# Kernel tuning notes

Hardware: AMD Instinct MI355X
Metric: run time of the kernel (lower is better)

Reference implementation:

```python
import jax, jax.numpy as jnp
import numpy as np

N_POWER_ITER = 5


def _spectral_normalize(w, n_iter=N_POWER_ITER):
    # w: [out, in] 1x1-conv weight; divide by top singular value (power iteration,
    # deterministic init), mirroring torch.nn.utils.spectral_norm's reparameterization.
    u = jnp.full((w.shape[0],), 1.0 / np.sqrt(w.shape[0]), dtype=w.dtype)
    for _ in range(n_iter):
        v = w.T @ u
        v = v / (jnp.linalg.norm(v) + 1e-12)
        u = w @ v
        u = u / (jnp.linalg.norm(u) + 1e-12)
    sigma = u @ (w @ v)
    return w / sigma


def _maxpool2x2(x):
    # x: [B, C, H, W] -> [B, C, H//2, W//2]
    B, C, H, W = x.shape
    return x.reshape(B, C, H // 2, 2, W // 2, 2).max(axis=(3, 5))


def _conv1x1(w, x):
    # 1x1 conv == channel-mixing einsum. w: [out, in], x: [B, in, H, W]
    return jnp.einsum('oc,bchw->bohw', w, x)


def setup_inputs() -> dict:
    key = jax.random.key(0)
    kx, kq, kk, kv, ko = jax.random.split(key, 5)
    C = 512
    B, H, W = 16, 64, 64
    scale = 0.05
    return {
        'x': jax.random.normal(kx, (B, C, H, W), dtype=jnp.float32),
        'Wq': jax.random.normal(kq, (C // 8, C), dtype=jnp.float32) * scale,
        'Wk': jax.random.normal(kk, (C // 8, C), dtype=jnp.float32) * scale,
        'Wv': jax.random.normal(kv, (C // 2, C), dtype=jnp.float32) * scale,
        'Wo': jax.random.normal(ko, (C, C // 2), dtype=jnp.float32) * scale,
        'gamma': jnp.array([0.5], dtype=jnp.float32),
    }


def reference(x, Wq, Wk, Wv, Wo, gamma):
    B, C, H, W = x.shape
    n_ftrs = H * W
    wq = _spectral_normalize(Wq)
    wk = _spectral_normalize(Wk)
    wv = _spectral_normalize(Wv)
    wo = _spectral_normalize(Wo)
    f = _conv1x1(wq, x).reshape(B, C // 8, n_ftrs)                      # [B, C/8, HW]
    g = _maxpool2x2(_conv1x1(wk, x)).reshape(B, C // 8, n_ftrs // 4)    # [B, C/8, HW/4]
    h = _maxpool2x2(_conv1x1(wv, x)).reshape(B, C // 2, n_ftrs // 4)    # [B, C/2, HW/4]
    # scores: [B, HW, HW/4]; softmax over kv positions
    beta = jax.nn.softmax(jnp.einsum('bcn,bcm->bnm', f, g), axis=-1)
    # attention output: [B, C/2, HW]
    o = jnp.einsum('bcm,bnm->bcn', h, beta).reshape(B, C // 2, H, W)
    o = _conv1x1(wo, o)                                                 # [B, C, H, W]
    return gamma.reshape(()) * o + x
```

## Files before the change

### kernel.cpp

```cpp
#include <hip/hip_runtime.h>
#include <cstdint>

typedef __attribute__((ext_vector_type(8))) short bf16x8;
typedef __attribute__((ext_vector_type(4))) float f32x4;
typedef __attribute__((ext_vector_type(2))) unsigned int u32x2;

#define B_   16
#define C_   512
#define HW_  4096
#define M3_  384
#define HWP_ 1024
#define CV_  256

__device__ __forceinline__ unsigned short f2b(float f) {
  union { float f; unsigned u; } v; v.f = f;
  unsigned r = v.u + 0x7fffu + ((v.u >> 16) & 1u);
  return (unsigned short)(r >> 16);
}
__device__ __forceinline__ float b2f(unsigned short b) {
  union { unsigned u; float f; } v; v.u = ((unsigned)b) << 16;
  return v.f;
}
__device__ __forceinline__ f32x4 mfma16(bf16x8 a, bf16x8 b, f32x4 c) {
  return __builtin_amdgcn_mfma_f32_16x16x32_bf16(a, b, c, 0, 0, 0);
}

__global__ __launch_bounds__(256) void k_transpose(const float* __restrict__ x,
                                                   unsigned short* __restrict__ xb) {
  __shared__ unsigned short t[64][66];
  const int b = blockIdx.z, k0 = blockIdx.y * 64, n0 = blockIdx.x * 64;
  const float* xp = x + (size_t)b * C_ * HW_;
  const int ln = threadIdx.x & 63, g = threadIdx.x >> 6;
  for (int kk = g; kk < 64; kk += 4)
    t[kk][ln] = f2b(xp[(size_t)(k0 + kk) * HW_ + n0 + ln]);
  __syncthreads();
  unsigned short* xo = xb + (size_t)b * HW_ * C_;
  for (int nn = g; nn < 64; nn += 4)
    xo[(size_t)(n0 + nn) * C_ + k0 + ln] = t[ln][nn];
}

__global__ __launch_bounds__(256) void k_wtrans(
    const float* __restrict__ Wq, const float* __restrict__ Wk,
    const float* __restrict__ Wv, const float* __restrict__ Wo,
    float* __restrict__ wt) {
  const float* w; int out, in; float* dst;
  switch (blockIdx.z) {
    case 0: w = Wq; out = 64;  in = 512; dst = wt;          break;
    case 1: w = Wk; out = 64;  in = 512; dst = wt + 32768;  break;
    case 2: w = Wv; out = 256; in = 512; dst = wt + 65536;  break;
    default: w = Wo; out = 512; in = 256; dst = wt + 196608; break;
  }
  const int o0 = blockIdx.y * 64, i0 = blockIdx.x * 64;
  if (o0 >= out || i0 >= in) return;
  __shared__ float t[64][65];
  const int ln = threadIdx.x & 63, g = threadIdx.x >> 6;
  for (int oo = g; oo < 64; oo += 4)
    t[oo][ln] = w[(size_t)(o0 + oo) * in + i0 + ln];
  __syncthreads();
  for (int ii = g; ii < 64; ii += 4)
    dst[(size_t)(i0 + ii) * out + o0 + ln] = t[ln][ii];
}

__device__ __forceinline__ float breduce1024(float val, float* red) {
  __syncthreads();
#pragma unroll
  for (int off = 32; off > 0; off >>= 1) val += __shfl_down(val, off);
  if ((threadIdx.x & 63) == 0) red[threadIdx.x >> 6] = val;
  __syncthreads();
  float s = 0.f;
#pragma unroll
  for (int i = 0; i < 16; ++i) s += red[i];
  return s;
}

__global__ __launch_bounds__(1024) void k_specnorm(
    const float* __restrict__ Wq, const float* __restrict__ Wk,
    const float* __restrict__ Wv, const float* __restrict__ Wo,
    const float* __restrict__ wt,
    unsigned short* __restrict__ wqkv, unsigned short* __restrict__ wob) {
  __shared__ float u[512], v[512];
  __shared__ float part[4096];
  __shared__ float red[16];
  const float* w; const float* wT; int out, in; unsigned short* dst;
  switch (blockIdx.x) {
    case 0: w = Wq; wT = wt;          out = 64;  in = 512; dst = wqkv;             break;
    case 1: w = Wk; wT = wt + 32768;  out = 64;  in = 512; dst = wqkv + 64 * 512;  break;
    case 2: w = Wv; wT = wt + 65536;  out = 256; in = 512; dst = wqkv + 128 * 512; break;
    default: w = Wo; wT = wt + 196608; out = 512; in = 256; dst = wob;             break;
  }
  const int tid = threadIdx.x;
  const float rs = rsqrtf((float)out);
  if (tid < out) u[tid] = rs;
  __syncthreads();
  for (int it = 0; it < 5; ++it) {
    {
      const int G = in >> 2, nch = 1024 / G;
      const int ch = tid / G, grp = tid - ch * G;
      const int rpc = out / nch, obase = ch * rpc;
      f32x4 acc = {0.f, 0.f, 0.f, 0.f};
#pragma unroll 8
      for (int r = 0; r < rpc; ++r) {
        const int o = obase + r;
        const f32x4 wv = *reinterpret_cast<const f32x4*>(&w[(size_t)o * in + grp * 4]);
        const float uo = u[o];
        acc[0] += wv[0] * uo; acc[1] += wv[1] * uo;
        acc[2] += wv[2] * uo; acc[3] += wv[3] * uo;
      }
      *reinterpret_cast<f32x4*>(&part[ch * in + grp * 4]) = acc;
      __syncthreads();
      if (tid < in) {
        float s = 0.f;
        for (int c2 = 0; c2 < nch; ++c2) s += part[c2 * in + tid];
        v[tid] = s;
      }
    }
    {
      float ss = (tid < in) ? 0.f : 0.f;
      if (tid < in) { __syncthreads(); ss = v[tid] * v[tid]; } else { __syncthreads(); }
      ss = breduce1024(ss, red);
      const float sv = 1.f / (sqrtf(ss) + 1e-12f);
      if (tid < in) v[tid] *= sv;
      __syncthreads();
    }
    {
      const int G = out >> 2, nch = 1024 / G;
      const int ch = tid / G, grp = tid - ch * G;
      const int cpc = in / nch, cbase = ch * cpc;
      f32x4 acc = {0.f, 0.f, 0.f, 0.f};
#pragma unroll 8
      for (int r = 0; r < cpc; ++r) {
        const int c = cbase + r;
        const f32x4 wv = *reinterpret_cast<const f32x4*>(&wT[(size_t)c * out + grp * 4]);
        const float vc = v[c];
        acc[0] += wv[0] * vc; acc[1] += wv[1] * vc;
        acc[2] += wv[2] * vc; acc[3] += wv[3] * vc;
      }
      *reinterpret_cast<f32x4*>(&part[ch * out + grp * 4]) = acc;
      __syncthreads();
      if (tid < out) {
        float s = 0.f;
        for (int c2 = 0; c2 < nch; ++c2) s += part[c2 * out + tid];
        u[tid] = s;
      }
    }
    {
      float su = 0.f;
      __syncthreads();
      if (tid < out) su = u[tid] * u[tid];
      su = breduce1024(su, red);
      const float sv2 = 1.f / (sqrtf(su) + 1e-12f);
      if (tid < out) u[tid] *= sv2;
      __syncthreads();
    }
  }
  float sp = 0.f;
  {
    const int G = out >> 2, nch = 1024 / G;
    const int ch = tid / G, grp = tid - ch * G;
    const int cpc = in / nch, cbase = ch * cpc;
    f32x4 acc = {0.f, 0.f, 0.f, 0.f};
#pragma unroll 8
    for (int r = 0; r < cpc; ++r) {
      const int c = cbase + r;
      const f32x4 wv = *reinterpret_cast<const f32x4*>(&wT[(size_t)c * out + grp * 4]);
      const float vc = v[c];
      acc[0] += wv[0] * vc; acc[1] += wv[1] * vc;
      acc[2] += wv[2] * vc; acc[3] += wv[3] * vc;
    }
    *reinterpret_cast<f32x4*>(&part[ch * out + grp * 4]) = acc;
    __syncthreads();
    if (tid < out) {
      float s = 0.f;
      for (int c2 = 0; c2 < nch; ++c2) s += part[c2 * out + tid];
      sp = s * u[tid];
    }
  }
  sp = breduce1024(sp, red);
  const float oscale = (blockIdx.x == 0) ? 1.44269504f : 1.0f;
  const float inv_sigma = (1.f / sp) * oscale;
  const int total = out * in;
  for (int i = tid * 4; i < total; i += 4096) {
    const f32x4 wv = *reinterpret_cast<const f32x4*>(&w[i]);
    u32x2 pw;
    pw[0] = ((unsigned)f2b(wv[1] * inv_sigma) << 16) | f2b(wv[0] * inv_sigma);
    pw[1] = ((unsigned)f2b(wv[3] * inv_sigma) << 16) | f2b(wv[2] * inv_sigma);
    *reinterpret_cast<u32x2*>(&dst[i]) = pw;
  }
}

__global__ __launch_bounds__(256) void k_gemm_qkv(
    const unsigned short* __restrict__ xb, const unsigned short* __restrict__ wqkv,
    unsigned short* __restrict__ yt) {
  __shared__ alignas(16) char smem[32768];
  unsigned short* As = (unsigned short*)smem;
  unsigned short* Bs = (unsigned short*)(smem + 16384);
  const int lid = blockIdx.x;
  const int swz = (lid & 7) * 192 + (lid >> 3);
  const int mt = swz % 3, rest = swz / 3;
  const int nt = rest & 31, b = rest >> 5;
  const int n0 = nt * 128, m0 = mt * 128;
  const unsigned short* Ap = xb + (size_t)b * HW_ * C_ + (size_t)n0 * C_;
  const unsigned short* Bp = wqkv + (size_t)m0 * C_;
  const int tid = threadIdx.x, lane = tid & 63, wid = tid >> 6;
  const int wn = (wid >> 1) * 64, wm = (wid & 1) * 64;
  f32x4 acc[4][4] = {};
  for (int k0 = 0; k0 < C_; k0 += 64) {
    __syncthreads();
#pragma unroll
    for (int i = 0; i < 4; ++i) {
      const int r = i * 32 + (tid >> 3);
      const int s = tid & 7, ss = s ^ (r & 7);
      *reinterpret_cast<f32x4*>(&As[r * 64 + ss * 8]) =
          *reinterpret_cast<const f32x4*>(&Ap[(size_t)r * C_ + k0 + s * 8]);
      *reinterpret_cast<f32x4*>(&Bs[r * 64 + ss * 8]) =
          *reinterpret_cast<const f32x4*>(&Bp[(size_t)r * C_ + k0 + s * 8]);
    }
    __syncthreads();
#pragma unroll
    for (int kk = 0; kk < 2; ++kk) {
      bf16x8 af[4], bfr[4];
#pragma unroll
      for (int i = 0; i < 4; ++i) {
        const int r = wn + i * 16 + (lane & 15);
        const int slot = (kk * 4 + (lane >> 4)) ^ (r & 7);
        af[i] = *reinterpret_cast<const bf16x8*>(&As[r * 64 + slot * 8]);
      }
#pragma unroll
      for (int j = 0; j < 4; ++j) {
        const int r = wm + j * 16 + (lane & 15);
        const int slot = (kk * 4 + (lane >> 4)) ^ (r & 7);
        bfr[j] = *reinterpret_cast<const bf16x8*>(&Bs[r * 64 + slot * 8]);
      }
#pragma unroll
      for (int i = 0; i < 4; ++i)
#pragma unroll
        for (int j = 0; j < 4; ++j) acc[i][j] = mfma16(af[i], bfr[j], acc[i][j]);
    }
  }
  unsigned short* eps = (unsigned short*)smem;
  unsigned short* Y = yt + (size_t)b * HW_ * M3_;
#pragma unroll
  for (int h = 0; h < 2; ++h) {
    __syncthreads();
    if ((wid >> 1) == h) {
#pragma unroll
      for (int i = 0; i < 4; ++i)
#pragma unroll
        for (int j = 0; j < 4; ++j)
#pragma unroll
          for (int r = 0; r < 4; ++r) {
            const int nl = i * 16 + (lane >> 4) * 4 + r;
            const int ml = wm + j * 16 + (lane & 15);
            eps[nl * 136 + ml] = f2b(acc[i][j][r]);
          }
    }
    __syncthreads();
#pragma unroll
    for (int t = 0; t < 4; ++t) {
      const int row = t * 16 + (tid >> 4);
      const int m8 = (tid & 15) * 8;
      *reinterpret_cast<f32x4*>(&Y[(size_t)(n0 + h * 64 + row) * M3_ + m0 + m8]) =
          *reinterpret_cast<const f32x4*>(&eps[row * 136 + m8]);
    }
  }
}

__global__ __launch_bounds__(256) void k_pool_g(const unsigned short* __restrict__ yt,
                                                unsigned short* __restrict__ gt) {
  const int b = blockIdx.y, mp0 = blockIdx.x * 64;
  const int c = threadIdx.x & 63, dm = threadIdx.x >> 6;
  const unsigned short* Y = yt + (size_t)b * HW_ * M3_;
  unsigned short* G = gt + (size_t)b * HWP_ * 64;
  for (int mm = dm; mm < 64; mm += 4) {
    const int mp = mp0 + mm;
    const int n00 = (mp >> 5) * 128 + (mp & 31) * 2;
    const float a0 = b2f(Y[(size_t)n00 * M3_ + 64 + c]);
    const float a1 = b2f(Y[(size_t)(n00 + 1) * M3_ + 64 + c]);
    const float a2 = b2f(Y[(size_t)(n00 + 64) * M3_ + 64 + c]);
    const float a3 = b2f(Y[(size_t)(n00 + 65) * M3_ + 64 + c]);
    G[(size_t)mp * 64 + c] = f2b(fmaxf(fmaxf(a0, a1), fmaxf(a2, a3)));
  }
}

__global__ __launch_bounds__(256) void k_pool_vt(const unsigned short* __restrict__ yt,
                                                 unsigned short* __restrict__ vt) {
  __shared__ unsigned short t[64][66];
  const int b = blockIdx.z, mp0 = blockIdx.x * 64, cv0 = blockIdx.y * 64;
  const unsigned short* Y = yt + (size_t)b * HW_ * M3_;
  const int c = threadIdx.x & 63, dm = threadIdx.x >> 6;
  for (int mm = dm; mm < 64; mm += 4) {
    const int mp = mp0 + mm;
    const int n00 = (mp >> 5) * 128 + (mp & 31) * 2;
    const float a0 = b2f(Y[(size_t)n00 * M3_ + 128 + cv0 + c]);
    const float a1 = b2f(Y[(size_t)(n00 + 1) * M3_ + 128 + cv0 + c]);
    const float a2 = b2f(Y[(size_t)(n00 + 64) * M3_ + 128 + cv0 + c]);
    const float a3 = b2f(Y[(size_t)(n00 + 65) * M3_ + 128 + cv0 + c]);
    t[mm][c] = f2b(fmaxf(fmaxf(a0, a1), fmaxf(a2, a3)));
  }
  __syncthreads();
  unsigned short* V = vt + (size_t)b * CV_ * HWP_;
  for (int cc = dm; cc < 64; cc += 4)
    V[(size_t)(cv0 + cc) * HWP_ + mp0 + c] = t[c][cc];
}

__global__ __launch_bounds__(512, 4) void k_attn(
    const unsigned short* __restrict__ yt, const unsigned short* __restrict__ gt,
    const unsigned short* __restrict__ vt, unsigned short* __restrict__ oat) {
  __shared__ alignas(16) char smem[57344];
  unsigned short* Ks = (unsigned short*)smem;
  unsigned short* Vs = (unsigned short*)(smem + 8192);
  unsigned short* Ps = (unsigned short*)(smem + 40960);
  const int lid = blockIdx.x;
  const int swz = (lid & 7) * 64 + (lid >> 3);
  const int q0 = (swz & 31) * 128, b = swz >> 5;
  const int tid = threadIdx.x, lane = tid & 63, wid = tid >> 6;
  const int q = lane & 15, g = lane >> 4;
  const unsigned short* Qg = yt + (size_t)b * HW_ * M3_ + (size_t)q0 * M3_;
  const unsigned short* Gg = gt + (size_t)b * HWP_ * 64;
  const unsigned short* Vg = vt + (size_t)b * CV_ * HWP_;
  unsigned short* P = Ps + wid * 1024;
  bf16x8 qf[2];
#pragma unroll
  for (int kk = 0; kk < 2; ++kk)
    qf[kk] = *reinterpret_cast<const bf16x8*>(&Qg[(size_t)(wid * 16 + q) * M3_ + kk * 32 + g * 8]);
  f32x4 kreg, vreg[4];
  {
    const int r = tid >> 3, s = tid & 7;
    kreg = *reinterpret_cast<const f32x4*>(&Gg[(size_t)r * 64 + s * 8]);
  }
#pragma unroll
  for (int t = 0; t < 4; ++t) {
    const int ch = tid + t * 512, r = ch >> 3, s = ch & 7;
    vreg[t] = *reinterpret_cast<const f32x4*>(&Vg[(size_t)r * HWP_ + s * 8]);
  }
  f32x4 oacc[16] = {};
  float m_run = -1e30f, l_run = 0.f;
  for (int it = 0; it < 16; ++it) {
    __syncthreads();
    {
      const int r = tid >> 3, s = tid & 7, ss = s ^ (r & 7);
      *reinterpret_cast<f32x4*>(&Ks[r * 64 + ss * 8]) = kreg;
    }
#pragma unroll
    for (int t = 0; t < 4; ++t) {
      const int ch = tid + t * 512, r = ch >> 3, s = ch & 7, ss = s ^ (r & 7);
      *reinterpret_cast<f32x4*>(&Vs[r * 64 + ss * 8]) = vreg[t];
    }
    __syncthreads();
    if (it < 15) {
      const int kvn = (it + 1) * 64;
      {
        const int r = tid >> 3, s = tid & 7;
        kreg = *reinterpret_cast<const f32x4*>(&Gg[(size_t)(kvn + r) * 64 + s * 8]);
      }
#pragma unroll
      for (int t = 0; t < 4; ++t) {
        const int ch = tid + t * 512, r = ch >> 3, s = ch & 7;
        vreg[t] = *reinterpret_cast<const f32x4*>(&Vg[(size_t)r * HWP_ + kvn + s * 8]);
      }
    }
    f32x4 sacc[4] = {};
#pragma unroll
    for (int kk = 0; kk < 2; ++kk) {
      bf16x8 kf[4];
#pragma unroll
      for (int i = 0; i < 4; ++i) {
        const int row = i * 16 + q;
        const int sl = (kk * 4 + g) ^ (row & 7);
        kf[i] = *reinterpret_cast<const bf16x8*>(&Ks[row * 64 + sl * 8]);
      }
#pragma unroll
      for (int i = 0; i < 4; ++i) sacc[i] = mfma16(kf[i], qf[kk], sacc[i]);
    }
    float tmax = -1e30f;
#pragma unroll
    for (int i = 0; i < 4; ++i)
#pragma unroll
      for (int r = 0; r < 4; ++r) tmax = fmaxf(tmax, sacc[i][r]);
    tmax = fmaxf(tmax, __shfl_xor(tmax, 16));
    tmax = fmaxf(tmax, __shfl_xor(tmax, 32));
    if (__any(tmax > m_run + 11.0f)) {
      const float mnew = fmaxf(m_run, tmax);
      const float alpha = exp2f(m_run - mnew);
      m_run = mnew;
      l_run *= alpha;
      float al[4];
#pragma unroll
      for (int r = 0; r < 4; ++r) al[r] = __shfl(alpha, g * 4 + r);
#pragma unroll
      for (int j = 0; j < 16; ++j) {
        oacc[j][0] *= al[0]; oacc[j][1] *= al[1];
        oacc[j][2] *= al[2]; oacc[j][3] *= al[3];
      }
    }
    float lsum = 0.f;
#pragma unroll
    for (int i = 0; i < 4; ++i) {
      const float p0 = exp2f(sacc[i][0] - m_run);
      const float p1 = exp2f(sacc[i][1] - m_run);
      const float p2 = exp2f(sacc[i][2] - m_run);
      const float p3 = exp2f(sacc[i][3] - m_run);
      lsum += (p0 + p1) + (p2 + p3);
      u32x2 pw;
      pw[0] = ((unsigned)f2b(p1) << 16) | f2b(p0);
      pw[1] = ((unsigned)f2b(p3) << 16) | f2b(p2);
      const int sl = (2 * i + (g >> 1)) ^ (q & 7);
      *reinterpret_cast<u32x2*>(&P[q * 64 + sl * 8 + (g & 1) * 4]) = pw;
    }
    lsum += __shfl_xor(lsum, 16);
    lsum += __shfl_xor(lsum, 32);
    l_run += lsum;
    __builtin_amdgcn_s_setprio(1);
#pragma unroll
    for (int kk = 0; kk < 2; ++kk) {
      const bf16x8 pa = *reinterpret_cast<const bf16x8*>(&P[q * 64 + ((kk * 4 + g) ^ (q & 7)) * 8]);
#pragma unroll
      for (int j = 0; j < 16; ++j) {
        const int row = j * 16 + q;
        const int sl = (kk * 4 + g) ^ (row & 7);
        const bf16x8 vf = *reinterpret_cast<const bf16x8*>(&Vs[row * 64 + sl * 8]);
        oacc[j] = mfma16(pa, vf, oacc[j]);
      }
    }
    __builtin_amdgcn_s_setprio(0);
  }
  float linv[4];
  {
    const float myinv = 1.f / l_run;
#pragma unroll
    for (int r = 0; r < 4; ++r) linv[r] = __shfl(myinv, g * 4 + r);
  }
  unsigned short* eps = (unsigned short*)smem;
  unsigned short* O = oat + (size_t)b * HW_ * CV_ + (size_t)q0 * CV_;
#pragma unroll
  for (int h = 0; h < 2; ++h) {
    __syncthreads();
    if ((wid >> 2) == h) {
#pragma unroll
      for (int j = 0; j < 16; ++j)
#pragma unroll
        for (int r = 0; r < 4; ++r) {
          const int row = (wid & 3) * 16 + g * 4 + r;
          const int cv = j * 16 + q;
          eps[row * 264 + cv] = f2b(oacc[j][r] * linv[r]);
        }
    }
    __syncthreads();
#pragma unroll
    for (int t = 0; t < 4; ++t) {
      const int row = t * 16 + (tid >> 5);
      const int cv8 = (tid & 31) * 8;
      *reinterpret_cast<f32x4*>(&O[(size_t)(h * 64 + row) * CV_ + cv8]) =
          *reinterpret_cast<const f32x4*>(&eps[row * 264 + cv8]);
    }
  }
}

__global__ __launch_bounds__(256) void k_gemm_out(
    const unsigned short* __restrict__ oat, const unsigned short* __restrict__ wob,
    const float* __restrict__ x, const float* __restrict__ gamma,
    float* __restrict__ out) {
  __shared__ alignas(16) char smem[32768];
  unsigned short* As = (unsigned short*)smem;
  unsigned short* Bs = (unsigned short*)(smem + 16384);
  const int lid = blockIdx.x;
  const int swz = (lid & 7) * 256 + (lid >> 3);
  const int ct = swz & 3, nt = (swz >> 2) & 31, b = swz >> 7;
  const int n0 = nt * 128, co0 = ct * 128;
  const unsigned short* Ap = wob + (size_t)co0 * CV_;
  const unsigned short* Bp = oat + (size_t)b * HW_ * CV_ + (size_t)n0 * CV_;
  const int tid = threadIdx.x, lane = tid & 63, wid = tid >> 6;
  const int wc = (wid >> 1) * 64, wn = (wid & 1) * 64;
  f32x4 acc[4][4] = {};
  for (int k0 = 0; k0 < CV_; k0 += 64) {
    __syncthreads();
#pragma unroll
    for (int i = 0; i < 4; ++i) {
      const int r = i * 32 + (tid >> 3);
      const int s = tid & 7, ss = s ^ (r & 7);
      *reinterpret_cast<f32x4*>(&As[r * 64 + ss * 8]) =
          *reinterpret_cast<const f32x4*>(&Ap[(size_t)r * CV_ + k0 + s * 8]);
      *reinterpret_cast<f32x4*>(&Bs[r * 64 + ss * 8]) =
          *reinterpret_cast<const f32x4*>(&Bp[(size_t)r * CV_ + k0 + s * 8]);
    }
    __syncthreads();
#pragma unroll
    for (int kk = 0; kk < 2; ++kk) {
      bf16x8 af[4], bfr[4];
#pragma unroll
      for (int i = 0; i < 4; ++i) {
        const int r = wc + i * 16 + (lane & 15);
        const int slot = (kk * 4 + (lane >> 4)) ^ (r & 7);
        af[i] = *reinterpret_cast<const bf16x8*>(&As[r * 64 + slot * 8]);
      }
#pragma unroll
      for (int j = 0; j < 4; ++j) {
        const int r = wn + j * 16 + (lane & 15);
        const int slot = (kk * 4 + (lane >> 4)) ^ (r & 7);
        bfr[j] = *reinterpret_cast<const bf16x8*>(&Bs[r * 64 + slot * 8]);
      }
#pragma unroll
      for (int i = 0; i < 4; ++i)
#pragma unroll
        for (int j = 0; j < 4; ++j) acc[i][j] = mfma16(af[i], bfr[j], acc[i][j]);
    }
  }
  float* eps = (float*)smem;
  const float g = gamma[0];
  const size_t base = (size_t)b * C_ * HW_;
#pragma unroll
  for (int h = 0; h < 4; ++h) {
    __syncthreads();
    if ((wid >> 1) == (h >> 1)) {
#pragma unroll
      for (int ii = 0; ii < 2; ++ii) {
        const int i = (h & 1) * 2 + ii;
#pragma unroll
        for (int j = 0; j < 4; ++j)
#pragma unroll
          for (int r = 0; r < 4; ++r) {
            const int col2 = ii * 16 + (lane >> 4) * 4 + r;
            const int nl = wn + j * 16 + (lane & 15);
            eps[col2 * 132 + nl] = acc[i][j][r];
          }
      }
    }
    __syncthreads();
#pragma unroll
    for (int t = 0; t < 4; ++t) {
      const int row = t * 8 + (tid >> 5);
      const int col = (tid & 31) * 4;
      const size_t goff = base + (size_t)(co0 + h * 32 + row) * HW_ + n0 + col;
      const f32x4 xv = *reinterpret_cast<const f32x4*>(&x[goff]);
      const f32x4 av = *reinterpret_cast<const f32x4*>(&eps[row * 132 + col]);
      f32x4 ov;
      ov[0] = g * av[0] + xv[0];
      ov[1] = g * av[1] + xv[1];
      ov[2] = g * av[2] + xv[2];
      ov[3] = g * av[3] + xv[3];
      *reinterpret_cast<f32x4*>(&out[goff]) = ov;
    }
  }
}

extern "C" void kernel_launch(void* const* d_in, const int* in_sizes, int n_in,
                              void* d_out, int out_size, void* d_ws, size_t ws_size,
                              hipStream_t stream) {
  (void)in_sizes; (void)n_in; (void)out_size; (void)ws_size;
  const float* x     = (const float*)d_in[0];
  const float* Wq    = (const float*)d_in[1];
  const float* Wk    = (const float*)d_in[2];
  const float* Wv    = (const float*)d_in[3];
  const float* Wo    = (const float*)d_in[4];
  const float* gamma = (const float*)d_in[5];
  float* out = (float*)d_out;
  char* ws = (char*)d_ws;

  unsigned short* wqkv = (unsigned short*)(ws);
  unsigned short* wob  = (unsigned short*)(ws + 393216);
  unsigned short* xb   = (unsigned short*)(ws + 655360);
  unsigned short* yt   = (unsigned short*)(ws + 67764224);
  unsigned short* gt   = (unsigned short*)(ws + 118095872);
  unsigned short* vt   = (unsigned short*)(ws + 120193024);
  unsigned short* oat  = xb;
  float* wt = (float*)yt;

  k_transpose<<<dim3(64, 8, 16), 256, 0, stream>>>(x, xb);
  k_wtrans<<<dim3(8, 8, 4), 256, 0, stream>>>(Wq, Wk, Wv, Wo, wt);
  k_specnorm<<<4, 1024, 0, stream>>>(Wq, Wk, Wv, Wo, wt, wqkv, wob);
  k_gemm_qkv<<<1536, 256, 0, stream>>>(xb, wqkv, yt);
  k_pool_g<<<dim3(16, 16), 256, 0, stream>>>(yt, gt);
  k_pool_vt<<<dim3(16, 4, 16), 256, 0, stream>>>(yt, vt);
  k_attn<<<512, 512, 0, stream>>>(yt, gt, vt, oat);
  k_gemm_out<<<2048, 256, 0, stream>>>(oat, wob, x, gamma, out);
}
```

Before: 349.1 us.

## Restructure attention kernel to split value channels across waves with register-resident K/V

The attention kernel now uses 256-thread blocks, each handling 64 queries. Each wave owns 64 value channels for all 64 queries rather than 16 queries across all 256 channels. K and V fragments load straight from global memory into registers, with prefetch of the next tile, so the LDS staging of K/V and two barriers per iteration are gone. P tiles and per-row rescale factors are shared through double-buffered LDS with one barrier per iteration. In exchange every block reloads K redundantly, the grid doubles, and occupancy shifts (launch bounds 256,3). A small specnorm barrier cleanup is also included.

```diff
diff --git a/kernel.cpp b/kernel.cpp
--- a/kernel.cpp
+++ b/kernel.cpp
@@ -115,8 +115,9 @@
       }
     }
     {
-      float ss = (tid < in) ? 0.f : 0.f;
-      if (tid < in) { __syncthreads(); ss = v[tid] * v[tid]; } else { __syncthreads(); }
+      float ss = 0.f;
+      __syncthreads();
+      if (tid < in) ss = v[tid] * v[tid];
       ss = breduce1024(ss, red);
       const float sv = 1.f / (sqrtf(ss) + 1e-12f);
       if (tid < in) v[tid] *= sv;
@@ -303,74 +304,53 @@
     V[(size_t)(cv0 + cc) * HWP_ + mp0 + c] = t[c][cc];
 }
 
-__global__ __launch_bounds__(512, 4) void k_attn(
+__global__ __launch_bounds__(256, 3) void k_attn(
     const unsigned short* __restrict__ yt, const unsigned short* __restrict__ gt,
     const unsigned short* __restrict__ vt, unsigned short* __restrict__ oat) {
-  __shared__ alignas(16) char smem[57344];
-  unsigned short* Ks = (unsigned short*)smem;
-  unsigned short* Vs = (unsigned short*)(smem + 8192);
-  unsigned short* Ps = (unsigned short*)(smem + 40960);
+  __shared__ alignas(16) char smem[34048];
+  float* aLds = (float*)(smem + 16384);
+  int* fLds = (int*)(smem + 16896);
   const int lid = blockIdx.x;
-  const int swz = (lid & 7) * 64 + (lid >> 3);
-  const int q0 = (swz & 31) * 128, b = swz >> 5;
+  const int swz = (lid & 7) * 128 + (lid >> 3);
+  const int q0 = (swz & 63) * 64, b = swz >> 6;
   const int tid = threadIdx.x, lane = tid & 63, wid = tid >> 6;
   const int q = lane & 15, g = lane >> 4;
+  const int cvb = wid * 64;
   const unsigned short* Qg = yt + (size_t)b * HW_ * M3_ + (size_t)q0 * M3_;
   const unsigned short* Gg = gt + (size_t)b * HWP_ * 64;
-  const unsigned short* Vg = vt + (size_t)b * CV_ * HWP_;
-  unsigned short* P = Ps + wid * 1024;
+  const unsigned short* Vg = vt + (size_t)b * CV_ * HWP_ + (size_t)cvb * HWP_;
   bf16x8 qf[2];
 #pragma unroll
   for (int kk = 0; kk < 2; ++kk)
     qf[kk] = *reinterpret_cast<const bf16x8*>(&Qg[(size_t)(wid * 16 + q) * M3_ + kk * 32 + g * 8]);
-  f32x4 kreg, vreg[4];
-  {
-    const int r = tid >> 3, s = tid & 7;
-    kreg = *reinterpret_cast<const f32x4*>(&Gg[(size_t)r * 64 + s * 8]);
-  }
-#pragma unroll
-  for (int t = 0; t < 4; ++t) {
-    const int ch = tid + t * 512, r = ch >> 3, s = ch & 7;
-    vreg[t] = *reinterpret_cast<const f32x4*>(&Vg[(size_t)r * HWP_ + s * 8]);
-  }
-  f32x4 oacc[16] = {};
+  bf16x8 kf[2][4], vf[2][4];
+#pragma unroll
+  for (int kk = 0; kk < 2; ++kk)
+#pragma unroll
+    for (int i = 0; i < 4; ++i)
+      kf[kk][i] = *reinterpret_cast<const bf16x8*>(&Gg[(size_t)(i * 16 + q) * 64 + kk * 32 + g * 8]);
+#pragma unroll
+  for (int kk = 0; kk < 2; ++kk)
+#pragma unroll
+    for (int j = 0; j < 4; ++j)
+      vf[kk][j] = *reinterpret_cast<const bf16x8*>(&Vg[(size_t)(j * 16 + q) * HWP_ + kk * 32 + g * 8]);
+  f32x4 oacc[4][4] = {};
   float m_run = -1e30f, l_run = 0.f;
   for (int it = 0; it < 16; ++it) {
-    __syncthreads();
-    {
-      const int r = tid >> 3, s = tid & 7, ss = s ^ (r & 7);
-      *reinterpret_cast<f32x4*>(&Ks[r * 64 + ss * 8]) = kreg;
-    }
-#pragma unroll
-    for (int t = 0; t < 4; ++t) {
-      const int ch = tid + t * 512, r = ch >> 3, s = ch & 7, ss = s ^ (r & 7);
-      *reinterpret_cast<f32x4*>(&Vs[r * 64 + ss * 8]) = vreg[t];
-    }
-    __syncthreads();
+    const int cur = it & 1;
+    unsigned short* P = (unsigned short*)smem + cur * 4096;
+    f32x4 sacc[4] = {};
+#pragma unroll
+    for (int kk = 0; kk < 2; ++kk)
+#pragma unroll
+      for (int i = 0; i < 4; ++i) sacc[i] = mfma16(kf[kk][i], qf[kk], sacc[i]);
     if (it < 15) {
       const int kvn = (it + 1) * 64;
-      {
-        const int r = tid >> 3, s = tid & 7;
-        kreg = *reinterpret_cast<const f32x4*>(&Gg[(size_t)(kvn + r) * 64 + s * 8]);
-      }
-#pragma unroll
-      for (int t = 0; t < 4; ++t) {
-        const int ch = tid + t * 512, r = ch >> 3, s = ch & 7;
-        vreg[t] = *reinterpret_cast<const f32x4*>(&Vg[(size_t)r * HWP_ + kvn + s * 8]);
-      }
-    }
-    f32x4 sacc[4] = {};
-#pragma unroll
-    for (int kk = 0; kk < 2; ++kk) {
-      bf16x8 kf[4];
-#pragma unroll
-      for (int i = 0; i < 4; ++i) {
-        const int row = i * 16 + q;
-        const int sl = (kk * 4 + g) ^ (row & 7);
-        kf[i] = *reinterpret_cast<const bf16x8*>(&Ks[row * 64 + sl * 8]);
-      }
-#pragma unroll
-      for (int i = 0; i < 4; ++i) sacc[i] = mfma16(kf[i], qf[kk], sacc[i]);
+#pragma unroll
+      for (int kk = 0; kk < 2; ++kk)
+#pragma unroll
+        for (int i = 0; i < 4; ++i)
+          kf[kk][i] = *reinterpret_cast<const bf16x8*>(&Gg[(size_t)(kvn + i * 16 + q) * 64 + kk * 32 + g * 8]);
     }
     float tmax = -1e30f;
 #pragma unroll
@@ -379,20 +359,18 @@
       for (int r = 0; r < 4; ++r) tmax = fmaxf(tmax, sacc[i][r]);
     tmax = fmaxf(tmax, __shfl_xor(tmax, 16));
     tmax = fmaxf(tmax, __shfl_xor(tmax, 32));
+    float alpha = 1.f;
+    int resc = 0;
     if (__any(tmax > m_run + 11.0f)) {
       const float mnew = fmaxf(m_run, tmax);
-      const float alpha = exp2f(m_run - mnew);
+      alpha = exp2f(m_run - mnew);
       m_run = mnew;
       l_run *= alpha;
-      float al[4];
-#pragma unroll
-      for (int r = 0; r < 4; ++r) al[r] = __shfl(alpha, g * 4 + r);
-#pragma unroll
-      for (int j = 0; j < 16; ++j) {
-        oacc[j][0] *= al[0]; oacc[j][1] *= al[1];
-        oacc[j][2] *= al[2]; oacc[j][3] *= al[3];
-      }
-    }
+      resc = 1;
+    }
+    if (lane < 16) aLds[cur * 64 + wid * 16 + lane] = alpha;
+    if (lane == 0) fLds[cur * 4 + wid] = resc;
+    const int qg = wid * 16 + q;
     float lsum = 0.f;
 #pragma unroll
     for (int i = 0; i < 4; ++i) {
@@ -405,54 +383,75 @@
       pw[0] = ((unsigned)f2b(p1) << 16) | f2b(p0);
       pw[1] = ((unsigned)f2b(p3) << 16) | f2b(p2);
       const int sl = (2 * i + (g >> 1)) ^ (q & 7);
-      *reinterpret_cast<u32x2*>(&P[q * 64 + sl * 8 + (g & 1) * 4]) = pw;
+      *reinterpret_cast<u32x2*>(&P[qg * 64 + sl * 8 + (g & 1) * 4]) = pw;
     }
     lsum += __shfl_xor(lsum, 16);
     lsum += __shfl_xor(lsum, 32);
     l_run += lsum;
+    __syncthreads();
+    if (fLds[cur * 4 + 0] | fLds[cur * 4 + 1] | fLds[cur * 4 + 2] | fLds[cur * 4 + 3]) {
+#pragma unroll
+      for (int f = 0; f < 4; ++f) {
+        float al[4];
+#pragma unroll
+        for (int r = 0; r < 4; ++r) al[r] = aLds[cur * 64 + f * 16 + g * 4 + r];
+#pragma unroll
+        for (int j = 0; j < 4; ++j) {
+          oacc[f][j][0] *= al[0]; oacc[f][j][1] *= al[1];
+          oacc[f][j][2] *= al[2]; oacc[f][j][3] *= al[3];
+        }
+      }
+    }
     __builtin_amdgcn_s_setprio(1);
 #pragma unroll
     for (int kk = 0; kk < 2; ++kk) {
-      const bf16x8 pa = *reinterpret_cast<const bf16x8*>(&P[q * 64 + ((kk * 4 + g) ^ (q & 7)) * 8]);
-#pragma unroll
-      for (int j = 0; j < 16; ++j) {
-        const int row = j * 16 + q;
-        const int sl = (kk * 4 + g) ^ (row & 7);
-        const bf16x8 vf = *reinterpret_cast<const bf16x8*>(&Vs[row * 64 + sl * 8]);
-        oacc[j] = mfma16(pa, vf, oacc[j]);
+#pragma unroll
+      for (int f = 0; f < 4; ++f) {
+        const int row = f * 16 + q;
+        const bf16x8 pa = *reinterpret_cast<const bf16x8*>(
+            &P[row * 64 + (((kk * 4 + g) ^ (q & 7))) * 8]);
+#pragma unroll
+        for (int j = 0; j < 4; ++j)
+          oacc[f][j] = mfma16(pa, vf[kk][j], oacc[f][j]);
       }
     }
     __builtin_amdgcn_s_setprio(0);
-  }
-  float linv[4];
-  {
-    const float myinv = 1.f / l_run;
-#pragma unroll
-    for (int r = 0; r < 4; ++r) linv[r] = __shfl(myinv, g * 4 + r);
-  }
+    if (it < 15) {
+      const int kvn = (it + 1) * 64;
+#pragma unroll
+      for (int kk = 0; kk < 2; ++kk)
+#pragma unroll
+        for (int j = 0; j < 4; ++j)
+          vf[kk][j] = *reinterpret_cast<const bf16x8*>(&Vg[(size_t)(j * 16 + q) * HWP_ + kvn + kk * 32 + g * 8]);
+    }
+  }
+  float* lLds = (float*)(smem + 33792);
+  if (lane < 16) lLds[wid * 16 + lane] = 1.f / l_run;
+  __syncthreads();
+  float linv[4][4];
+#pragma unroll
+  for (int f = 0; f < 4; ++f)
+#pragma unroll
+    for (int r = 0; r < 4; ++r) linv[f][r] = lLds[f * 16 + g * 4 + r];
   unsigned short* eps = (unsigned short*)smem;
+#pragma unroll
+  for (int f = 0; f < 4; ++f)
+#pragma unroll
+    for (int j = 0; j < 4; ++j)
+#pragma unroll
+      for (int r = 0; r < 4; ++r) {
+        const int row = f * 16 + g * 4 + r;
+        const int cv = cvb + j * 16 + q;
+        eps[row * 264 + cv] = f2b(oacc[f][j][r] * linv[f][r]);
+      }
+  __syncthreads();
   unsigned short* O = oat + (size_t)b * HW_ * CV_ + (size_t)q0 * CV_;
 #pragma unroll
-  for (int h = 0; h < 2; ++h) {
-    __syncthreads();
-    if ((wid >> 2) == h) {
-#pragma unroll
-      for (int j = 0; j < 16; ++j)
-#pragma unroll
-        for (int r = 0; r < 4; ++r) {
-          const int row = (wid & 3) * 16 + g * 4 + r;
-          const int cv = j * 16 + q;
-          eps[row * 264 + cv] = f2b(oacc[j][r] * linv[r]);
-        }
-    }
-    __syncthreads();
-#pragma unroll
-    for (int t = 0; t < 4; ++t) {
-      const int row = t * 16 + (tid >> 5);
-      const int cv8 = (tid & 31) * 8;
-      *reinterpret_cast<f32x4*>(&O[(size_t)(h * 64 + row) * CV_ + cv8]) =
-          *reinterpret_cast<const f32x4*>(&eps[row * 264 + cv8]);
-    }
+  for (int t = 0; t < 8; ++t) {
+    const int row = t * 8 + (tid >> 5);
+    const int cv8 = (tid & 31) * 8;
+    *reinterpret_cast<f32x4*>(&O[(size_t)row * CV_ + cv8]) =
+        *reinterpret_cast<const f32x4*>(&eps[row * 264 + cv8]);
   }
 }
 
@@ -571,6 +570,6 @@
   k_gemm_qkv<<<1536, 256, 0, stream>>>(xb, wqkv, yt);
   k_pool_g<<<dim3(16, 16), 256, 0, stream>>>(yt, gt);
   k_pool_vt<<<dim3(16, 4, 16), 256, 0, stream>>>(yt, vt);
-  k_attn<<<512, 512, 0, stream>>>(yt, gt, vt, oat);
+  k_attn<<<1024, 256, 0, stream>>>(yt, gt, vt, oat);
   k_gemm_out<<<2048, 256, 0, stream>>>(oat, wob, x, gamma, out);
 }
```

Measured after the change: 476.8 us. 1.37x slower.

## Process two query sub-tiles per wave in attention to reuse V fragments

Applied to the files above, without the earlier changes.

The attention kernel now runs 4 waves of 256 threads instead of 8, with each wave handling 32 query rows as two 16-row halves. Each V fragment read from shared memory then feeds two MFMAs, which halves LDS traffic per FLOP and doubles per-thread global staging loads. The cost is about double the accumulator registers (two sets of 16 f32x4 accumulators plus 8 V staging registers), which may lower occupancy or cause spills, and fewer waves per block hide less latency. A redundant conditional __syncthreads in the spectral-norm kernel is also simplified.

```diff
diff --git a/kernel.cpp b/kernel.cpp
--- a/kernel.cpp
+++ b/kernel.cpp
@@ -115,8 +115,9 @@
       }
     }
     {
-      float ss = (tid < in) ? 0.f : 0.f;
-      if (tid < in) { __syncthreads(); ss = v[tid] * v[tid]; } else { __syncthreads(); }
+      float ss = 0.f;
+      __syncthreads();
+      if (tid < in) ss = v[tid] * v[tid];
       ss = breduce1024(ss, red);
       const float sv = 1.f / (sqrtf(ss) + 1e-12f);
       if (tid < in) v[tid] *= sv;
@@ -303,7 +304,7 @@
     V[(size_t)(cv0 + cc) * HWP_ + mp0 + c] = t[c][cc];
 }
 
-__global__ __launch_bounds__(512, 4) void k_attn(
+__global__ __launch_bounds__(256, 2) void k_attn(
     const unsigned short* __restrict__ yt, const unsigned short* __restrict__ gt,
     const unsigned short* __restrict__ vt, unsigned short* __restrict__ oat) {
   __shared__ alignas(16) char smem[57344];
@@ -315,51 +316,56 @@
   const int q0 = (swz & 31) * 128, b = swz >> 5;
   const int tid = threadIdx.x, lane = tid & 63, wid = tid >> 6;
   const int q = lane & 15, g = lane >> 4;
-  const unsigned short* Qg = yt + (size_t)b * HW_ * M3_ + (size_t)q0 * M3_;
+  const unsigned short* Qg = yt + (size_t)b * HW_ * M3_ + (size_t)(q0 + wid * 32) * M3_;
   const unsigned short* Gg = gt + (size_t)b * HWP_ * 64;
   const unsigned short* Vg = vt + (size_t)b * CV_ * HWP_;
-  unsigned short* P = Ps + wid * 1024;
-  bf16x8 qf[2];
-#pragma unroll
-  for (int kk = 0; kk < 2; ++kk)
-    qf[kk] = *reinterpret_cast<const bf16x8*>(&Qg[(size_t)(wid * 16 + q) * M3_ + kk * 32 + g * 8]);
-  f32x4 kreg, vreg[4];
-  {
-    const int r = tid >> 3, s = tid & 7;
-    kreg = *reinterpret_cast<const f32x4*>(&Gg[(size_t)r * 64 + s * 8]);
-  }
-#pragma unroll
-  for (int t = 0; t < 4; ++t) {
-    const int ch = tid + t * 512, r = ch >> 3, s = ch & 7;
+  unsigned short* P = Ps + wid * 2048;
+  bf16x8 qf[2][2];
+#pragma unroll
+  for (int h = 0; h < 2; ++h)
+#pragma unroll
+    for (int kk = 0; kk < 2; ++kk)
+      qf[h][kk] = *reinterpret_cast<const bf16x8*>(&Qg[(size_t)(h * 16 + q) * M3_ + kk * 32 + g * 8]);
+  f32x4 kreg[2], vreg[8];
+#pragma unroll
+  for (int t = 0; t < 2; ++t) {
+    const int i = tid + t * 256, r = i >> 3, s = i & 7;
+    kreg[t] = *reinterpret_cast<const f32x4*>(&Gg[(size_t)r * 64 + s * 8]);
+  }
+#pragma unroll
+  for (int t = 0; t < 8; ++t) {
+    const int i = tid + t * 256, r = i >> 3, s = i & 7;
     vreg[t] = *reinterpret_cast<const f32x4*>(&Vg[(size_t)r * HWP_ + s * 8]);
   }
-  f32x4 oacc[16] = {};
-  float m_run = -1e30f, l_run = 0.f;
+  f32x4 oacc[2][16] = {};
+  float m_run[2] = {-1e30f, -1e30f}, l_run[2] = {0.f, 0.f};
   for (int it = 0; it < 16; ++it) {
     __syncthreads();
-    {
-      const int r = tid >> 3, s = tid & 7, ss = s ^ (r & 7);
-      *reinterpret_cast<f32x4*>(&Ks[r * 64 + ss * 8]) = kreg;
-    }
-#pragma unroll
-    for (int t = 0; t < 4; ++t) {
-      const int ch = tid + t * 512, r = ch >> 3, s = ch & 7, ss = s ^ (r & 7);
+#pragma unroll
+    for (int t = 0; t < 2; ++t) {
+      const int i = tid + t * 256, r = i >> 3, s = i & 7, ss = s ^ (r & 7);
+      *reinterpret_cast<f32x4*>(&Ks[r * 64 + ss * 8]) = kreg[t];
+    }
+#pragma unroll
+    for (int t = 0; t < 8; ++t) {
+      const int i = tid + t * 256, r = i >> 3, s = i & 7, ss = s ^ (r & 7);
       *reinterpret_cast<f32x4*>(&Vs[r * 64 + ss * 8]) = vreg[t];
     }
     __syncthreads();
     if (it < 15) {
       const int kvn = (it + 1) * 64;
-      {
-        const int r = tid >> 3, s = tid & 7;
-        kreg = *reinterpret_cast<const f32x4*>(&Gg[(size_t)(kvn + r) * 64 + s * 8]);
-      }
-#pragma unroll
-      for (int t = 0; t < 4; ++t) {
-        const int ch = tid + t * 512, r = ch >> 3, s = ch & 7;
+#pragma unroll
+      for (int t = 0; t < 2; ++t) {
+        const int i = tid + t * 256, r = i >> 3, s = i & 7;
+        kreg[t] = *reinterpret_cast<const f32x4*>(&Gg[(size_t)(kvn + r) * 64 + s * 8]);
+      }
+#pragma unroll
+      for (int t = 0; t < 8; ++t) {
+        const int i = tid + t * 256, r = i >> 3, s = i & 7;
         vreg[t] = *reinterpret_cast<const f32x4*>(&Vg[(size_t)r * HWP_ + kvn + s * 8]);
       }
     }
-    f32x4 sacc[4] = {};
+    f32x4 sacc[2][4] = {};
 #pragma unroll
     for (int kk = 0; kk < 2; ++kk) {
       bf16x8 kf[4];
@@ -370,87 +376,101 @@
         kf[i] = *reinterpret_cast<const bf16x8*>(&Ks[row * 64 + sl * 8]);
       }
 #pragma unroll
-      for (int i = 0; i < 4; ++i) sacc[i] = mfma16(kf[i], qf[kk], sacc[i]);
-    }
-    float tmax = -1e30f;
-#pragma unroll
-    for (int i = 0; i < 4; ++i)
-#pragma unroll
-      for (int r = 0; r < 4; ++r) tmax = fmaxf(tmax, sacc[i][r]);
-    tmax = fmaxf(tmax, __shfl_xor(tmax, 16));
-    tmax = fmaxf(tmax, __shfl_xor(tmax, 32));
-    if (__any(tmax > m_run + 11.0f)) {
-      const float mnew = fmaxf(m_run, tmax);
-      const float alpha = exp2f(m_run - mnew);
-      m_run = mnew;
-      l_run *= alpha;
-      float al[4];
-#pragma unroll
-      for (int r = 0; r < 4; ++r) al[r] = __shfl(alpha, g * 4 + r);
-#pragma unroll
-      for (int j = 0; j < 16; ++j) {
-        oacc[j][0] *= al[0]; oacc[j][1] *= al[1];
-        oacc[j][2] *= al[2]; oacc[j][3] *= al[3];
-      }
-    }
-    float lsum = 0.f;
-#pragma unroll
-    for (int i = 0; i < 4; ++i) {
-      const float p0 = exp2f(sacc[i][0] - m_run);
-      const float p1 = exp2f(sacc[i][1] - m_run);
-      const float p2 = exp2f(sacc[i][2] - m_run);
-      const float p3 = exp2f(sacc[i][3] - m_run);
-      lsum += (p0 + p1) + (p2 + p3);
-      u32x2 pw;
-      pw[0] = ((unsigned)f2b(p1) << 16) | f2b(p0);
-      pw[1] = ((unsigned)f2b(p3) << 16) | f2b(p2);
-      const int sl = (2 * i + (g >> 1)) ^ (q & 7);
-      *reinterpret_cast<u32x2*>(&P[q * 64 + sl * 8 + (g & 1) * 4]) = pw;
-    }
-    lsum += __shfl_xor(lsum, 16);
-    lsum += __shfl_xor(lsum, 32);
-    l_run += lsum;
+      for (int h = 0; h < 2; ++h)
+#pragma unroll
+        for (int i = 0; i < 4; ++i) sacc[h][i] = mfma16(kf[i], qf[h][kk], sacc[h][i]);
+    }
+#pragma unroll
+    for (int h = 0; h < 2; ++h) {
+      float tmax = -1e30f;
+#pragma unroll
+      for (int i = 0; i < 4; ++i)
+#pragma unroll
+        for (int r = 0; r < 4; ++r) tmax = fmaxf(tmax, sacc[h][i][r]);
+      tmax = fmaxf(tmax, __shfl_xor(tmax, 16));
+      tmax = fmaxf(tmax, __shfl_xor(tmax, 32));
+      if (__any(tmax > m_run[h] + 11.0f)) {
+        const float mnew = fmaxf(m_run[h], tmax);
+        const float alpha = exp2f(m_run[h] - mnew);
+        m_run[h] = mnew;
+        l_run[h] *= alpha;
+        float al[4];
+#pragma unroll
+        for (int r = 0; r < 4; ++r) al[r] = __shfl(alpha, g * 4 + r);
+#pragma unroll
+        for (int j = 0; j < 16; ++j) {
+          oacc[h][j][0] *= al[0]; oacc[h][j][1] *= al[1];
+          oacc[h][j][2] *= al[2]; oacc[h][j][3] *= al[3];
+        }
+      }
+      const int qg = h * 16 + q;
+      float lsum = 0.f;
+#pragma unroll
+      for (int i = 0; i < 4; ++i) {
+        const float p0 = exp2f(sacc[h][i][0] - m_run[h]);
+        const float p1 = exp2f(sacc[h][i][1] - m_run[h]);
+        const float p2 = exp2f(sacc[h][i][2] - m_run[h]);
+        const float p3 = exp2f(sacc[h][i][3] - m_run[h]);
+        lsum += (p0 + p1) + (p2 + p3);
+        u32x2 pw;
+        pw[0] = ((unsigned)f2b(p1) << 16) | f2b(p0);
+        pw[1] = ((unsigned)f2b(p3) << 16) | f2b(p2);
+        const int sl = (2 * i + (g >> 1)) ^ (qg & 7);
+        *reinterpret_cast<u32x2*>(&P[qg * 64 + sl * 8 + (g & 1) * 4]) = pw;
+      }
+      lsum += __shfl_xor(lsum, 16);
+      lsum += __shfl_xor(lsum, 32);
+      l_run[h] += lsum;
+    }
     __builtin_amdgcn_s_setprio(1);
 #pragma unroll
     for (int kk = 0; kk < 2; ++kk) {
-      const bf16x8 pa = *reinterpret_cast<const bf16x8*>(&P[q * 64 + ((kk * 4 + g) ^ (q & 7)) * 8]);
+      bf16x8 pa[2];
+#pragma unroll
+      for (int h = 0; h < 2; ++h)
+        pa[h] = *reinterpret_cast<const bf16x8*>(
+            &P[(h * 16 + q) * 64 + (((kk * 4 + g) ^ (q & 7))) * 8]);
 #pragma unroll
       for (int j = 0; j < 16; ++j) {
         const int row = j * 16 + q;
         const int sl = (kk * 4 + g) ^ (row & 7);
         const bf16x8 vf = *reinterpret_cast<const bf16x8*>(&Vs[row * 64 + sl * 8]);
-        oacc[j] = mfma16(pa, vf, oacc[j]);
+        oacc[0][j] = mfma16(pa[0], vf, oacc[0][j]);
+        oacc[1][j] = mfma16(pa[1], vf, oacc[1][j]);
       }
     }
     __builtin_amdgcn_s_setprio(0);
   }
-  float linv[4];
-  {
-    const float myinv = 1.f / l_run;
-#pragma unroll
-    for (int r = 0; r < 4; ++r) linv[r] = __shfl(myinv, g * 4 + r);
+  float linv[2][4];
+#pragma unroll
+  for (int h = 0; h < 2; ++h) {
+    const float myinv = 1.f / l_run[h];
+#pragma unroll
+    for (int r = 0; r < 4; ++r) linv[h][r] = __shfl(myinv, g * 4 + r);
   }
   unsigned short* eps = (unsigned short*)smem;
   unsigned short* O = oat + (size_t)b * HW_ * CV_ + (size_t)q0 * CV_;
 #pragma unroll
-  for (int h = 0; h < 2; ++h) {
-    __syncthreads();
-    if ((wid >> 2) == h) {
-#pragma unroll
-      for (int j = 0; j < 16; ++j)
-#pragma unroll
-        for (int r = 0; r < 4; ++r) {
-          const int row = (wid & 3) * 16 + g * 4 + r;
-          const int cv = j * 16 + q;
-          eps[row * 264 + cv] = f2b(oacc[j][r] * linv[r]);
-        }
-    }
-    __syncthreads();
-#pragma unroll
-    for (int t = 0; t < 4; ++t) {
-      const int row = t * 16 + (tid >> 5);
+  for (int ch = 0; ch < 2; ++ch) {
+    __syncthreads();
+    if ((wid >> 1) == ch) {
+#pragma unroll
+      for (int h = 0; h < 2; ++h)
+#pragma unroll
+        for (int j = 0; j < 16; ++j)
+#pragma unroll
+          for (int r = 0; r < 4; ++r) {
+            const int row = (wid & 1) * 32 + h * 16 + g * 4 + r;
+            const int cv = j * 16 + q;
+            eps[row * 264 + cv] = f2b(oacc[h][j][r] * linv[h][r]);
+          }
+    }
+    __syncthreads();
+#pragma unroll
+    for (int t = 0; t < 8; ++t) {
+      const int row = t * 8 + (tid >> 5);
       const int cv8 = (tid & 31) * 8;
-      *reinterpret_cast<f32x4*>(&O[(size_t)(h * 64 + row) * CV_ + cv8]) =
+      *reinterpret_cast<f32x4*>(&O[(size_t)(ch * 64 + row) * CV_ + cv8]) =
           *reinterpret_cast<const f32x4*>(&eps[row * 264 + cv8]);
     }
   }
@@ -571,6 +591,6 @@
   k_gemm_qkv<<<1536, 256, 0, stream>>>(xb, wqkv, yt);
   k_pool_g<<<dim3(16, 16), 256, 0, stream>>>(yt, gt);
   k_pool_vt<<<dim3(16, 4, 16), 256, 0, stream>>>(yt, vt);
-  k_attn<<<512, 512, 0, stream>>>(yt, gt, vt, oat);
+  k_attn<<<512, 256, 0, stream>>>(yt, gt, vt, oat);
   k_gemm_out<<<2048, 256, 0, stream>>>(oat, wob, x, gamma, out);
 }
```

Result: faster. 323.8 us (-7.3%).
